# Performance work log

Hardware: AMD Instinct MI355X
Metric: run time of the kernel (lower is better)

## Reference

```python
import jax, jax.numpy as jnp
import numpy as np

B, N, D, S, ITERS = 64, 4096, 256, 8, 3
EPS_ATTN = 1e-8
EPS_LN = 1e-5


def layernorm(x, g, b):
    mu = jnp.mean(x, axis=-1, keepdims=True)
    var = jnp.mean(jnp.square(x - mu), axis=-1, keepdims=True)
    return (x - mu) * jax.lax.rsqrt(var + EPS_LN) * g + b


def setup_inputs() -> dict:
    key = jax.random.key(0)
    ks = jax.random.split(key, 12)
    inputs = jax.random.normal(ks[0], (B, N, D), jnp.float32)
    mask = jax.random.randint(ks[1], (B, N), 0, 2) == 1  # bool, True = masked out
    # xavier-normal init for slots parameter [S, D]
    slots_init = jax.random.normal(ks[2], (S, D), jnp.float32) * np.sqrt(2.0 / (S + D))
    w_std = np.sqrt(1.0 / D)
    Wq = jax.random.normal(ks[3], (D, D), jnp.float32) * w_std
    bq = jnp.zeros((D,), jnp.float32)
    Wk = jax.random.normal(ks[4], (D, D), jnp.float32) * w_std
    bk = jnp.zeros((D,), jnp.float32)
    Wv = jax.random.normal(ks[5], (D, D), jnp.float32) * w_std
    bv = jnp.zeros((D,), jnp.float32)
    W1 = jax.random.normal(ks[6], (D, D), jnp.float32) * w_std
    b1 = jnp.zeros((D,), jnp.float32)
    W2 = jax.random.normal(ks[7], (D, D), jnp.float32) * w_std
    b2 = jnp.zeros((D,), jnp.float32)
    g_in, b_in = jnp.ones((D,)), jnp.zeros((D,))
    g_s, b_s = jnp.ones((D,)), jnp.zeros((D,))
    g_m, b_m = jnp.ones((D,)), jnp.zeros((D,))
    g_o, b_o = jnp.ones((D,)), jnp.zeros((D,))
    return {
        "inputs": inputs, "mask": mask, "slots_init": slots_init,
        "g_in": g_in, "b_in": b_in, "g_s": g_s, "b_s": b_s,
        "g_m": g_m, "b_m": b_m, "g_o": g_o, "b_o": b_o,
        "Wq": Wq, "bq": bq, "Wk": Wk, "bk": bk, "Wv": Wv, "bv": bv,
        "W1": W1, "b1": b1, "W2": W2, "b2": b2,
    }


def reference(inputs, mask, slots_init, g_in, b_in, g_s, b_s, g_m, b_m, g_o, b_o,
              Wq, bq, Wk, bk, Wv, bv, W1, b1, W2, b2):
    x = layernorm(inputs, g_in, b_in)            # [B,N,D]
    k = x @ Wk + bk                               # [B,N,D]
    v = x @ Wv + bv                               # [B,N,D]
    slots = jnp.broadcast_to(slots_init, (B, S, D))
    scale = D ** -0.5
    neg_max = -jnp.finfo(inputs.dtype).max
    for _ in range(ITERS):
        slots_prev = slots
        s = layernorm(slots, g_s, b_s)
        q = s @ Wq + bq                           # [B,S,D]
        dots = jnp.einsum('bid,bjd->bij', q, k) * scale   # [B,S,N]
        dots = jnp.where(mask[:, None, :], neg_max, dots)
        attn = jax.nn.softmax(dots, axis=1)       # softmax over slots (unusual axis)
        attn = attn / (jnp.sum(attn, axis=-1, keepdims=True) + EPS_ATTN)
        updates = jnp.einsum('bjd,bij->bid', v, attn)     # [B,S,D]
        slots = slots_prev + updates
        h = layernorm(slots, g_m, b_m)
        h = jax.nn.relu(h @ W1 + b1) @ W2 + b2    # 2-layer MLP
        slots = slots + h
    return layernorm(slots, g_o, b_o)
```

## Files before the change

### kernel.cpp

```cpp
#include <hip/hip_runtime.h>
#include <stdint.h>

#define BB 64
#define NN 4096
#define DD 256
#define SS 8
#define NITER 3
#define NCHUNK 8
#define EPS_LN 1e-5f
#define EPS_ATTN 1e-8f

typedef __attribute__((ext_vector_type(4))) float fvec4;
typedef __attribute__((ext_vector_type(8))) __bf16 bf16x8;
typedef __attribute__((ext_vector_type(8))) unsigned short usvec8;
typedef __attribute__((ext_vector_type(4))) unsigned short usvec4;

__device__ __forceinline__ float bf2f(unsigned short u) {
  return __uint_as_float(((unsigned)u) << 16);
}
__device__ __forceinline__ unsigned short f2bf(float f) {
  unsigned u = __float_as_uint(f);
  u += 0x7FFFu + ((u >> 16) & 1u);
  return (unsigned short)(u >> 16);
}
__device__ __forceinline__ void async_copy16(void* ldsp, const void* gp) {
  __builtin_amdgcn_global_load_lds(
      (const __attribute__((address_space(1))) unsigned int*)gp,
      (__attribute__((address_space(3))) unsigned int*)ldsp, 16, 0, 0);
}

__global__ void k_sinit(const float* __restrict__ slots_init, float* __restrict__ slots) {
  int b = blockIdx.x, t = threadIdx.x;
  const fvec4* src = (const fvec4*)slots_init;
  fvec4* dst = (fvec4*)(slots + (size_t)b * SS * DD);
  for (int j = t; j < SS * DD / 4; j += 256) dst[j] = src[j];
}

__global__ void k_wprepT(const float* __restrict__ Wk, float* __restrict__ WkT) {
  __shared__ float tile[16][17];
  int bx = blockIdx.x, by = blockIdx.y, t = threadIdx.x;
  int r = t >> 4, c = t & 15;
  tile[r][c] = Wk[(size_t)(by * 16 + r) * DD + bx * 16 + c];
  __syncthreads();
  WkT[(size_t)(bx * 16 + r) * DD + by * 16 + c] = tile[c][r];
}

__launch_bounds__(256)
__global__ void k_wcomb(const float* __restrict__ Wq, const float* __restrict__ WkT,
                        const float* __restrict__ bq, const float* __restrict__ bk,
                        float* __restrict__ Wqk, float* __restrict__ bqk,
                        float* __restrict__ wqbk, float* __restrict__ bqbk) {
  __shared__ float wqrow[DD];
  __shared__ float red[4];
  const float sc = 0.0625f;
  int j = blockIdx.x, t = threadIdx.x;
  wqrow[t] = Wq[(size_t)j * DD + t];
  __syncthreads();
  float a = 0.f;
#pragma unroll 4
  for (int dk = 0; dk < DD; dk++) a += wqrow[dk] * WkT[(size_t)dk * DD + t];
  Wqk[(size_t)j * DD + t] = a * sc;
  float c = wqrow[t] * bk[t];
#pragma unroll
  for (int m = 32; m >= 1; m >>= 1) c += __shfl_xor(c, m);
  if ((t & 63) == 0) red[t >> 6] = c;
  __syncthreads();
  if (t == 0) wqbk[j] = sc * (red[0] + red[1] + red[2] + red[3]);
  if (j == 0) {
    float bb = 0.f;
#pragma unroll 4
    for (int dk = 0; dk < DD; dk++) bb += bq[dk] * WkT[(size_t)dk * DD + t];
    bqk[t] = bb * sc;
    __syncthreads();
    float c2 = bq[t] * bk[t];
#pragma unroll
    for (int m = 32; m >= 1; m >>= 1) c2 += __shfl_xor(c2, m);
    if ((t & 63) == 0) red[t >> 6] = c2;
    __syncthreads();
    if (t == 0) bqbk[0] = sc * (red[0] + red[1] + red[2] + red[3]);
  }
}

__launch_bounds__(256)
__global__ void k_lnx(const float* __restrict__ in, const float* __restrict__ g,
                      const float* __restrict__ bt, unsigned short* __restrict__ xbf) {
  int t = threadIdx.x;
  long row = (long)blockIdx.x * 32 + (t >> 3);
  int u = t & 7;
  const float* rp = in + row * DD;
  fvec4 v[8];
  float s = 0.f, s2 = 0.f;
#pragma unroll
  for (int j = 0; j < 8; j++) {
    v[j] = *(const fvec4*)(rp + j * 32 + u * 4);
    s += v[j].x + v[j].y + v[j].z + v[j].w;
    s2 += v[j].x * v[j].x + v[j].y * v[j].y + v[j].z * v[j].z + v[j].w * v[j].w;
  }
  s += __shfl_xor(s, 1); s2 += __shfl_xor(s2, 1);
  s += __shfl_xor(s, 2); s2 += __shfl_xor(s2, 2);
  s += __shfl_xor(s, 4); s2 += __shfl_xor(s2, 4);
  float mu = s / DD;
  float rs = rsqrtf(s2 / DD - mu * mu + EPS_LN);
#pragma unroll
  for (int j = 0; j < 8; j++) {
    fvec4 gg = *(const fvec4*)(g + j * 32 + u * 4);
    fvec4 bb = *(const fvec4*)(bt + j * 32 + u * 4);
    usvec4 o;
    o[0] = f2bf((v[j].x - mu) * rs * gg.x + bb.x);
    o[1] = f2bf((v[j].y - mu) * rs * gg.y + bb.y);
    o[2] = f2bf((v[j].z - mu) * rs * gg.z + bb.z);
    o[3] = f2bf((v[j].w - mu) * rs * gg.w + bb.w);
    *(usvec4*)&xbf[row * DD + j * 32 + u * 4] = o;
  }
}

__launch_bounds__(256)
__global__ void k_slotq2(const float* __restrict__ slots, const float* __restrict__ g_s,
                         const float* __restrict__ b_s, const float* __restrict__ Wqk,
                         const float* __restrict__ bqk, const float* __restrict__ wqbk,
                         const float* __restrict__ bqbk, float* __restrict__ qk,
                         float* __restrict__ qb, float* __restrict__ colsum) {
  __shared__ float sl[SS][DD];
  __shared__ float part[4][SS][64];
  __shared__ float qbp[4][SS];
  int b = blockIdx.x, cg = blockIdx.y, t = threadIdx.x;
  if (cg == 0 && t < SS) colsum[b * SS + t] = 0.f;
  int row = t >> 5, seg = t & 31;
  {
    const float* sp = slots + (size_t)(b * SS + row) * DD + seg * 8;
    float v[8];
    float s = 0.f, s2 = 0.f;
#pragma unroll
    for (int e = 0; e < 8; e++) { v[e] = sp[e]; s += v[e]; s2 += v[e] * v[e]; }
#pragma unroll
    for (int m = 16; m >= 1; m >>= 1) { s += __shfl_xor(s, m); s2 += __shfl_xor(s2, m); }
    float mu = s / DD;
    float rs = rsqrtf(s2 / DD - mu * mu + EPS_LN);
#pragma unroll
    for (int e = 0; e < 8; e++) {
      int d = seg * 8 + e;
      sl[row][d] = (v[e] - mu) * rs * g_s[d] + b_s[d];
    }
  }
  __syncthreads();
  float wb = wqbk[t];
  float c8[SS];
#pragma unroll
  for (int i = 0; i < SS; i++) c8[i] = sl[i][t] * wb;
#pragma unroll
  for (int m = 32; m >= 1; m >>= 1)
#pragma unroll
    for (int i = 0; i < SS; i++) c8[i] += __shfl_xor(c8[i], m);
  if ((t & 63) == 0) {
#pragma unroll
    for (int i = 0; i < SS; i++) qbp[t >> 6][i] = c8[i];
  }
  int kq = t >> 6, c = t & 63;
  int colg = cg * 64 + c;
  float a[SS] = {};
  for (int kk = 0; kk < 64; kk++) {
    int k = kq * 64 + kk;
    float wv = Wqk[(size_t)k * DD + colg];
#pragma unroll
    for (int i = 0; i < SS; i++) a[i] += sl[i][k] * wv;
  }
#pragma unroll
  for (int i = 0; i < SS; i++) part[kq][i][c] = a[i];
  __syncthreads();
  int i0 = t >> 6;
#pragma unroll
  for (int ii = 0; ii < 2; ii++) {
    int i = i0 + ii * 4;
    float s = part[0][i][c] + part[1][i][c] + part[2][i][c] + part[3][i][c];
    qk[(size_t)(b * SS + i) * DD + colg] = s + bqk[colg];
  }
  if (cg == 0 && t < SS)
    qb[b * SS + t] = qbp[0][t] + qbp[1][t] + qbp[2][t] + qbp[3][t] + bqbk[0];
}

__launch_bounds__(256, 2)
__global__ void k_attn2(const unsigned short* __restrict__ xbf,
                        const float* __restrict__ qkb, const float* __restrict__ qb,
                        const int* __restrict__ mask,
                        float* __restrict__ colsum, float* __restrict__ upart) {
  __shared__ __attribute__((aligned(16))) unsigned short kt[2][64 * 256];
  __shared__ float aL[2][64 * 9];
  int b = blockIdx.y, chunk = blockIdx.x, t = threadIdx.x;
  int w = t >> 6, lane = t & 63;
  int n_base = chunk * 512;
  int cl15 = lane & 15, hg = lane >> 4;

  bf16x8 qf[8];
  {
    int qrow = cl15 < 8 ? cl15 : 0;
    const float* qp = qkb + (size_t)(b * SS + qrow) * DD;
#pragma unroll
    for (int kst = 0; kst < 8; kst++) {
      int d0 = kst * 32 + hg * 8;
      usvec8 uq;
      if (cl15 < 8) {
        fvec4 q0 = *(const fvec4*)(qp + d0);
        fvec4 q1 = *(const fvec4*)(qp + d0 + 4);
        uq[0] = f2bf(q0.x); uq[1] = f2bf(q0.y); uq[2] = f2bf(q0.z); uq[3] = f2bf(q0.w);
        uq[4] = f2bf(q1.x); uq[5] = f2bf(q1.y); uq[6] = f2bf(q1.z); uq[7] = f2bf(q1.w);
      } else {
        uq = (usvec8)0;
      }
      qf[kst] = __builtin_bit_cast(bf16x8, uq);
    }
  }
  float qadd[4];
#pragma unroll
  for (int e = 0; e < 4; e++) qadd[e] = qb[b * SS + (hg & 1) * 4 + e];

  float acc[SS][8] = {};
  float csum[4] = {};
  int ns = t >> 5;

  auto stage = [&](int c, int bb) {
    int r0 = n_base + c * 64;
#pragma unroll
    for (int j = 0; j < 8; j++) {
      int gidx = w * 512 + j * 64 + lane;
      int row = gidx >> 5, c16 = gidx & 31;
      async_copy16(&kt[bb][gidx * 8],
                   xbf + ((size_t)(b * NN + r0 + row)) * DD + ((c16 ^ (row & 7)) * 8));
    }
  };

  stage(0, 0);
  for (int c = 0; c < 8; c++) {
    int bb = c & 1, pb = c & 1;
    int r0 = n_base + c * 64;
    if (c < 7) {
      stage(c + 1, bb ^ 1);
      asm volatile("s_waitcnt vmcnt(8)" ::: "memory");
    } else {
      asm volatile("s_waitcnt vmcnt(0)" ::: "memory");
    }
    __builtin_amdgcn_sched_barrier(0);
    fvec4 S = {0.f, 0.f, 0.f, 0.f};
    int row_l = w * 16 + cl15;
#pragma unroll
    for (int kst = 0; kst < 8; kst++) {
      int c16 = (kst * 4 + hg) ^ (row_l & 7);
      bf16x8 bfk = *(const bf16x8*)&kt[bb][row_l * 256 + c16 * 8];
      S = __builtin_amdgcn_mfma_f32_16x16x32_bf16(qf[kst], bfk, S, 0, 0, 0);
    }
    S[0] += qadd[0]; S[1] += qadd[1]; S[2] += qadd[2]; S[3] += qadd[3];
    {
      float m4 = fmaxf(fmaxf(S[0], S[1]), fmaxf(S[2], S[3]));
      float mo = __shfl_xor(m4, 16);
      float mx = fmaxf(m4, mo);
      float e0 = __expf(S[0] - mx), e1 = __expf(S[1] - mx);
      float e2 = __expf(S[2] - mx), e3 = __expf(S[3] - mx);
      float s4 = e0 + e1 + e2 + e3;
      float so = __shfl_xor(s4, 16);
      float inv = 1.f / (s4 + so);
      int mk = mask[(size_t)b * NN + r0 + row_l];
      float a0 = mk ? 0.125f : e0 * inv;
      float a1 = mk ? 0.125f : e1 * inv;
      float a2 = mk ? 0.125f : e2 * inv;
      float a3 = mk ? 0.125f : e3 * inv;
      if (lane < 32) {
        csum[0] += a0; csum[1] += a1; csum[2] += a2; csum[3] += a3;
        float* ap = &aL[pb][(w * 16 + cl15) * 9 + hg * 4];
        ap[0] = a0; ap[1] = a1; ap[2] = a2; ap[3] = a3;
      }
    }
    __syncthreads();
#pragma unroll
    for (int s8 = 0; s8 < 8; s8++) {
      int r = s8 * 8 + ns;
      usvec8 vv = *(const usvec8*)&kt[bb][r * 256 + (((t & 31)) ^ (r & 7)) * 8];
      float vf[8];
#pragma unroll
      for (int e = 0; e < 8; e++) vf[e] = bf2f(vv[e]);
#pragma unroll
      for (int i = 0; i < SS; i++) {
        float aw = aL[pb][r * 9 + i];
#pragma unroll
        for (int e = 0; e < 8; e++) acc[i][e] += aw * vf[e];
      }
    }
    __syncthreads();
  }
#pragma unroll
  for (int m = 1; m <= 8; m <<= 1)
#pragma unroll
    for (int e = 0; e < 4; e++) csum[e] += __shfl_xor(csum[e], m);
  if (lane == 0) {
#pragma unroll
    for (int e = 0; e < 4; e++) atomicAdd(&colsum[b * SS + e], csum[e]);
  } else if (lane == 16) {
#pragma unroll
    for (int e = 0; e < 4; e++) atomicAdd(&colsum[b * SS + 4 + e], csum[e]);
  }
#pragma unroll
  for (int i = 0; i < SS; i++)
#pragma unroll
    for (int e = 0; e < 8; e++) acc[i][e] += __shfl_xor(acc[i][e], 32);
  __syncthreads();
  float* red = (float*)&kt[0][0];
  if (lane < 32) {
#pragma unroll
    for (int i = 0; i < SS; i++) {
      fvec4 a0 = {acc[i][0], acc[i][1], acc[i][2], acc[i][3]};
      fvec4 a1 = {acc[i][4], acc[i][5], acc[i][6], acc[i][7]};
      *(fvec4*)&red[(w * SS + i) * DD + lane * 8] = a0;
      *(fvec4*)&red[(w * SS + i) * DD + lane * 8 + 4] = a1;
    }
  }
  __syncthreads();
  int i2 = t >> 5, dsg = (t & 31) * 8;
  float* up = upart + ((size_t)(b * NCHUNK + chunk)) * (SS * DD) + i2 * DD + dsg;
#pragma unroll
  for (int e = 0; e < 8; e++)
    up[e] = red[(0 * SS + i2) * DD + dsg + e] + red[(1 * SS + i2) * DD + dsg + e] +
            red[(2 * SS + i2) * DD + dsg + e] + red[(3 * SS + i2) * DD + dsg + e];
}

__launch_bounds__(256)
__global__ void k_updv(const float* __restrict__ upart, const float* __restrict__ Wv,
                       const float* __restrict__ bv, const float* __restrict__ colsum,
                       float* __restrict__ upd) {
  __shared__ float yL[SS][DD];
  __shared__ float part[4][SS][64];
  int b = blockIdx.x, cg = blockIdx.y, t = threadIdx.x;
#pragma unroll
  for (int i = 0; i < SS; i++) {
    float s = 0.f;
#pragma unroll
    for (int c = 0; c < NCHUNK; c++)
      s += upart[((size_t)(b * NCHUNK + c)) * (SS * DD) + i * DD + t];
    yL[i][t] = s;
  }
  __syncthreads();
  int kq = t >> 6, c = t & 63;
  int colg = cg * 64 + c;
  float a[SS] = {};
  for (int kk = 0; kk < 64; kk++) {
    int k = kq * 64 + kk;
    float wv = Wv[(size_t)k * DD + colg];
#pragma unroll
    for (int i = 0; i < SS; i++) a[i] += yL[i][k] * wv;
  }
#pragma unroll
  for (int i = 0; i < SS; i++) part[kq][i][c] = a[i];
  __syncthreads();
  int i0 = t >> 6;
  float bvc = bv[colg];
#pragma unroll
  for (int ii = 0; ii < 2; ii++) {
    int i = i0 + ii * 4;
    float s = part[0][i][c] + part[1][i][c] + part[2][i][c] + part[3][i][c];
    upd[(size_t)(b * SS + i) * DD + colg] = s + bvc * colsum[b * SS + i];
  }
}

__launch_bounds__(256)
__global__ void k_mlp1(const float* __restrict__ slots, const float* __restrict__ colsum,
                       const float* __restrict__ upd, const float* __restrict__ g_m,
                       const float* __restrict__ b_m, const float* __restrict__ W1,
                       const float* __restrict__ b1, float* __restrict__ h2g,
                       float* __restrict__ snbuf) {
  __shared__ float hL[SS][DD];
  __shared__ float part[4][SS][64];
  int b = blockIdx.x, cg = blockIdx.y, t = threadIdx.x;
  int row = t >> 5, seg = t & 31;
  {
    float inv = 1.0f / (colsum[b * SS + row] + EPS_ATTN);
    const float* sp = slots + (size_t)(b * SS + row) * DD + seg * 8;
    const float* up = upd + (size_t)(b * SS + row) * DD + seg * 8;
    float v[8];
    float s = 0.f, s2 = 0.f;
#pragma unroll
    for (int e = 0; e < 8; e++) {
      v[e] = sp[e] + up[e] * inv;
      s += v[e]; s2 += v[e] * v[e];
    }
    if (cg == 0) {
      float* snp = snbuf + (size_t)(b * SS + row) * DD + seg * 8;
#pragma unroll
      for (int e = 0; e < 8; e++) snp[e] = v[e];
    }
#pragma unroll
    for (int m = 16; m >= 1; m >>= 1) { s += __shfl_xor(s, m); s2 += __shfl_xor(s2, m); }
    float mu = s / DD;
    float rs = rsqrtf(s2 / DD - mu * mu + EPS_LN);
#pragma unroll
    for (int e = 0; e < 8; e++) {
      int d = seg * 8 + e;
      hL[row][d] = (v[e] - mu) * rs * g_m[d] + b_m[d];
    }
  }
  __syncthreads();
  int kq = t >> 6, c = t & 63;
  int colg = cg * 64 + c;
  float a[SS] = {};
  for (int kk = 0; kk < 64; kk++) {
    int k = kq * 64 + kk;
    float wv = W1[(size_t)k * DD + colg];
#pragma unroll
    for (int i = 0; i < SS; i++) a[i] += hL[i][k] * wv;
  }
#pragma unroll
  for (int i = 0; i < SS; i++) part[kq][i][c] = a[i];
  __syncthreads();
  int i0 = t >> 6;
#pragma unroll
  for (int ii = 0; ii < 2; ii++) {
    int i = i0 + ii * 4;
    float s = part[0][i][c] + part[1][i][c] + part[2][i][c] + part[3][i][c];
    h2g[(size_t)(b * SS + i) * DD + colg] = fmaxf(s + b1[colg], 0.f);
  }
}

__launch_bounds__(256)
__global__ void k_mlp2(float* __restrict__ slots, const float* __restrict__ snbuf,
                       const float* __restrict__ h2g, const float* __restrict__ W2,
                       const float* __restrict__ b2) {
  __shared__ float h2L[SS][DD];
  __shared__ float part[4][SS][64];
  int b = blockIdx.x, cg = blockIdx.y, t = threadIdx.x;
  {
    const fvec4* src = (const fvec4*)(h2g + (size_t)b * SS * DD);
    fvec4* dst = (fvec4*)h2L;
    for (int j = t; j < SS * DD / 4; j += 256) dst[j] = src[j];
  }
  __syncthreads();
  int kq = t >> 6, c = t & 63;
  int colg = cg * 64 + c;
  float a[SS] = {};
  for (int kk = 0; kk < 64; kk++) {
    int k = kq * 64 + kk;
    float wv = W2[(size_t)k * DD + colg];
#pragma unroll
    for (int i = 0; i < SS; i++) a[i] += h2L[i][k] * wv;
  }
#pragma unroll
  for (int i = 0; i < SS; i++) part[kq][i][c] = a[i];
  __syncthreads();
  int i0 = t >> 6;
#pragma unroll
  for (int ii = 0; ii < 2; ii++) {
    int i = i0 + ii * 4;
    float s = part[0][i][c] + part[1][i][c] + part[2][i][c] + part[3][i][c];
    size_t idx = (size_t)(b * SS + i) * DD + colg;
    slots[idx] = snbuf[idx] + s + b2[colg];
  }
}

__launch_bounds__(256)
__global__ void k_out(const float* __restrict__ slots, const float* __restrict__ g_o,
                      const float* __restrict__ b_o, float* __restrict__ out) {
  int b = blockIdx.x, t = threadIdx.x;
  int row = t >> 5, seg = t & 31;
  const float* sp = slots + (size_t)(b * SS + row) * DD + seg * 8;
  float v[8];
  float s = 0.f, s2 = 0.f;
#pragma unroll
  for (int e = 0; e < 8; e++) { v[e] = sp[e]; s += v[e]; s2 += v[e] * v[e]; }
#pragma unroll
  for (int m = 16; m >= 1; m >>= 1) { s += __shfl_xor(s, m); s2 += __shfl_xor(s2, m); }
  float mu = s / DD;
  float rs = rsqrtf(s2 / DD - mu * mu + EPS_LN);
#pragma unroll
  for (int e = 0; e < 8; e++) {
    int d = seg * 8 + e;
    out[(size_t)(b * SS + row) * DD + d] = (v[e] - mu) * rs * g_o[d] + b_o[d];
  }
}

extern "C" void kernel_launch(void* const* d_in, const int* in_sizes, int n_in,
                              void* d_out, int out_size, void* d_ws, size_t ws_size,
                              hipStream_t stream) {
  (void)in_sizes; (void)n_in; (void)out_size; (void)ws_size;
  const float* inputs = (const float*)d_in[0];
  const int* mask = (const int*)d_in[1];
  const float* slots_init = (const float*)d_in[2];
  const float* g_in = (const float*)d_in[3];
  const float* b_in = (const float*)d_in[4];
  const float* g_s = (const float*)d_in[5];
  const float* b_s = (const float*)d_in[6];
  const float* g_m = (const float*)d_in[7];
  const float* b_m = (const float*)d_in[8];
  const float* g_o = (const float*)d_in[9];
  const float* b_o = (const float*)d_in[10];
  const float* Wq = (const float*)d_in[11];
  const float* bq = (const float*)d_in[12];
  const float* Wk = (const float*)d_in[13];
  const float* bk = (const float*)d_in[14];
  const float* Wv = (const float*)d_in[15];
  const float* bv = (const float*)d_in[16];
  const float* W1 = (const float*)d_in[17];
  const float* b1 = (const float*)d_in[18];
  const float* W2 = (const float*)d_in[19];
  const float* b2 = (const float*)d_in[20];
  float* out = (float*)d_out;

  char* ws = (char*)d_ws;
  size_t off = 0;
  auto alloc = [&](size_t bytes) -> void* {
    void* p = ws + off;
    off += (bytes + 255) & ~(size_t)255;
    return p;
  };
  unsigned short* xbf = (unsigned short*)alloc((size_t)BB * NN * DD * 2);
  float* WkT = (float*)alloc((size_t)DD * DD * 4);
  float* Wqk = (float*)alloc((size_t)DD * DD * 4);
  float* bqk = (float*)alloc((size_t)DD * 4);
  float* wqbk = (float*)alloc((size_t)DD * 4);
  float* bqbk = (float*)alloc(4);
  float* qk = (float*)alloc((size_t)BB * SS * DD * 4);
  float* qb = (float*)alloc((size_t)BB * SS * 4);
  float* slots = (float*)alloc((size_t)BB * SS * DD * 4);
  float* snbuf = (float*)alloc((size_t)BB * SS * DD * 4);
  float* h2g = (float*)alloc((size_t)BB * SS * DD * 4);
  float* upd = (float*)alloc((size_t)BB * SS * DD * 4);
  float* upart = (float*)alloc((size_t)BB * NCHUNK * SS * DD * 4);
  float* colsum = (float*)alloc((size_t)BB * SS * 4);

  k_sinit<<<dim3(BB), dim3(256), 0, stream>>>(slots_init, slots);
  k_wprepT<<<dim3(16, 16), dim3(256), 0, stream>>>(Wk, WkT);
  k_wcomb<<<dim3(DD), dim3(256), 0, stream>>>(Wq, WkT, bq, bk, Wqk, bqk, wqbk, bqbk);
  k_lnx<<<dim3(BB * NN / 32), dim3(256), 0, stream>>>(inputs, g_in, b_in, xbf);

  for (int it = 0; it < NITER; ++it) {
    k_slotq2<<<dim3(BB, 4), dim3(256), 0, stream>>>(slots, g_s, b_s, Wqk, bqk, wqbk, bqbk,
                                                    qk, qb, colsum);
    k_attn2<<<dim3(NCHUNK, BB), dim3(256), 0, stream>>>(xbf, qk, qb, mask, colsum, upart);
    k_updv<<<dim3(BB, 4), dim3(256), 0, stream>>>(upart, Wv, bv, colsum, upd);
    k_mlp1<<<dim3(BB, 4), dim3(256), 0, stream>>>(slots, colsum, upd, g_m, b_m, W1, b1, h2g, snbuf);
    k_mlp2<<<dim3(BB, 4), dim3(256), 0, stream>>>(slots, snbuf, h2g, W2, b2);
  }
  k_out<<<dim3(BB), dim3(256), 0, stream>>>(slots, g_o, b_o, out);
}
```

Measured before the change: 426.5 us.

## Fuse Wv projection, MLP and next-iteration query into one slot-side kernel

Replaces four per-iteration kernels (updv, mlp1, mlp2, slotq2) with a single k_slotside kernel launched on a (BB,4) grid. Each block redundantly computes the full Wv, W1 and W2 products for its batch entry, then the query projection for its column group. Slot and colsum buffers are double-buffered so that blocks can read the previous state while block cg==0 writes the new one. This removes three launches per iteration and the global round-trips of the intermediate buffers, at the cost of each of the four column blocks repeating the full 256x256 matvecs, which quadruples the weight reads and FLOPs for these stages.

```diff
diff --git a/kernel.cpp b/kernel.cpp
--- a/kernel.cpp
+++ b/kernel.cpp
@@ -321,12 +321,25 @@
 }
 
 __launch_bounds__(256)
-__global__ void k_updv(const float* __restrict__ upart, const float* __restrict__ Wv,
-                       const float* __restrict__ bv, const float* __restrict__ colsum,
-                       float* __restrict__ upd) {
+__global__ void k_slotside(const float* __restrict__ slots_rd, float* __restrict__ slots_wr,
+                           const float* __restrict__ upart,
+                           const float* __restrict__ Wv, const float* __restrict__ bv,
+                           const float* __restrict__ colsum_rd, float* __restrict__ colsum_wr,
+                           const float* __restrict__ g_m, const float* __restrict__ b_m,
+                           const float* __restrict__ W1, const float* __restrict__ b1,
+                           const float* __restrict__ W2, const float* __restrict__ b2,
+                           const float* __restrict__ g_s, const float* __restrict__ b_s,
+                           const float* __restrict__ Wqk, const float* __restrict__ bqk,
+                           const float* __restrict__ wqbk, const float* __restrict__ bqbk,
+                           float* __restrict__ qk, float* __restrict__ qb, int do_q) {
   __shared__ float yL[SS][DD];
-  __shared__ float part[4][SS][64];
+  __shared__ float snL[SS][DD];
+  __shared__ float hL[SS][DD];
+  __shared__ float h2L[SS][DD];
+  __shared__ float qbp[4][SS];
   int b = blockIdx.x, cg = blockIdx.y, t = threadIdx.x;
+  int row = t >> 5, seg = t & 31;
+  float cs[SS], csinv[SS];
 #pragma unroll
   for (int i = 0; i < SS; i++) {
     float s = 0.f;
@@ -335,120 +348,130 @@
       s += upart[((size_t)(b * NCHUNK + c)) * (SS * DD) + i * DD + t];
     yL[i][t] = s;
   }
-  __syncthreads();
-  int kq = t >> 6, c = t & 63;
-  int colg = cg * 64 + c;
-  float a[SS] = {};
-  for (int kk = 0; kk < 64; kk++) {
-    int k = kq * 64 + kk;
-    float wv = Wv[(size_t)k * DD + colg];
-#pragma unroll
-    for (int i = 0; i < SS; i++) a[i] += yL[i][k] * wv;
-  }
-#pragma unroll
-  for (int i = 0; i < SS; i++) part[kq][i][c] = a[i];
+#pragma unroll
+  for (int i = 0; i < SS; i++) {
+    cs[i] = colsum_rd[b * SS + i];
+    csinv[i] = 1.f / (cs[i] + EPS_ATTN);
+  }
+  __syncthreads();
+  {
+    float acc[SS] = {};
+    for (int k = 0; k < DD; k += 4) {
+      float w0 = Wv[(size_t)(k + 0) * DD + t];
+      float w1 = Wv[(size_t)(k + 1) * DD + t];
+      float w2 = Wv[(size_t)(k + 2) * DD + t];
+      float w3 = Wv[(size_t)(k + 3) * DD + t];
+#pragma unroll
+      for (int i = 0; i < SS; i++)
+        acc[i] += yL[i][k] * w0 + yL[i][k + 1] * w1 + yL[i][k + 2] * w2 + yL[i][k + 3] * w3;
+    }
+    float bvt = bv[t];
+#pragma unroll
+    for (int i = 0; i < SS; i++)
+      snL[i][t] = slots_rd[(size_t)(b * SS + i) * DD + t] + (acc[i] + bvt * cs[i]) * csinv[i];
+  }
+  __syncthreads();
+  {
+    float v[8], s = 0.f, s2 = 0.f;
+#pragma unroll
+    for (int e = 0; e < 8; e++) { v[e] = snL[row][seg * 8 + e]; s += v[e]; s2 += v[e] * v[e]; }
+#pragma unroll
+    for (int m = 16; m >= 1; m >>= 1) { s += __shfl_xor(s, m); s2 += __shfl_xor(s2, m); }
+    float mu = s / DD, rs = rsqrtf(s2 / DD - mu * mu + EPS_LN);
+#pragma unroll
+    for (int e = 0; e < 8; e++) {
+      int d = seg * 8 + e;
+      hL[row][d] = (v[e] - mu) * rs * g_m[d] + b_m[d];
+    }
+  }
+  __syncthreads();
+  {
+    float acc[SS] = {};
+    for (int k = 0; k < DD; k += 4) {
+      float w0 = W1[(size_t)(k + 0) * DD + t];
+      float w1 = W1[(size_t)(k + 1) * DD + t];
+      float w2 = W1[(size_t)(k + 2) * DD + t];
+      float w3 = W1[(size_t)(k + 3) * DD + t];
+#pragma unroll
+      for (int i = 0; i < SS; i++)
+        acc[i] += hL[i][k] * w0 + hL[i][k + 1] * w1 + hL[i][k + 2] * w2 + hL[i][k + 3] * w3;
+    }
+    float b1t = b1[t];
+#pragma unroll
+    for (int i = 0; i < SS; i++) h2L[i][t] = fmaxf(acc[i] + b1t, 0.f);
+  }
+  __syncthreads();
+  {
+    float acc[SS] = {};
+    for (int k = 0; k < DD; k += 4) {
+      float w0 = W2[(size_t)(k + 0) * DD + t];
+      float w1 = W2[(size_t)(k + 1) * DD + t];
+      float w2 = W2[(size_t)(k + 2) * DD + t];
+      float w3 = W2[(size_t)(k + 3) * DD + t];
+#pragma unroll
+      for (int i = 0; i < SS; i++)
+        acc[i] += h2L[i][k] * w0 + h2L[i][k + 1] * w1 + h2L[i][k + 2] * w2 + h2L[i][k + 3] * w3;
+    }
+    float b2t = b2[t];
+#pragma unroll
+    for (int i = 0; i < SS; i++) {
+      float v = snL[i][t] + acc[i] + b2t;
+      yL[i][t] = v;
+      if (cg == 0) slots_wr[(size_t)(b * SS + i) * DD + t] = v;
+    }
+  }
+  if (cg == 0 && t < SS) colsum_wr[b * SS + t] = 0.f;
+  if (!do_q) return;
+  __syncthreads();
+  {
+    float v[8], s = 0.f, s2 = 0.f;
+#pragma unroll
+    for (int e = 0; e < 8; e++) { v[e] = yL[row][seg * 8 + e]; s += v[e]; s2 += v[e] * v[e]; }
+#pragma unroll
+    for (int m = 16; m >= 1; m >>= 1) { s += __shfl_xor(s, m); s2 += __shfl_xor(s2, m); }
+    float mu = s / DD, rs = rsqrtf(s2 / DD - mu * mu + EPS_LN);
+#pragma unroll
+    for (int e = 0; e < 8; e++) {
+      int d = seg * 8 + e;
+      snL[row][d] = (v[e] - mu) * rs * g_s[d] + b_s[d];
+    }
+  }
+  __syncthreads();
+  float wb = wqbk[t];
+  float c8[SS];
+#pragma unroll
+  for (int i = 0; i < SS; i++) c8[i] = snL[i][t] * wb;
+#pragma unroll
+  for (int m = 32; m >= 1; m >>= 1)
+#pragma unroll
+    for (int i = 0; i < SS; i++) c8[i] += __shfl_xor(c8[i], m);
+  if ((t & 63) == 0) {
+#pragma unroll
+    for (int i = 0; i < SS; i++) qbp[t >> 6][i] = c8[i];
+  }
+  float(*part)[SS][64] = (float(*)[SS][64]) & hL[0][0];
+  int kq = t >> 6, c = t & 63, colg = cg * 64 + c;
+  {
+    float a[SS] = {};
+    for (int kk = 0; kk < 64; kk++) {
+      int k = kq * 64 + kk;
+      float wv = Wqk[(size_t)k * DD + colg];
+#pragma unroll
+      for (int i = 0; i < SS; i++) a[i] += snL[i][k] * wv;
+    }
+#pragma unroll
+    for (int i = 0; i < SS; i++) part[kq][i][c] = a[i];
+  }
   __syncthreads();
   int i0 = t >> 6;
-  float bvc = bv[colg];
 #pragma unroll
   for (int ii = 0; ii < 2; ii++) {
     int i = i0 + ii * 4;
     float s = part[0][i][c] + part[1][i][c] + part[2][i][c] + part[3][i][c];
-    upd[(size_t)(b * SS + i) * DD + colg] = s + bvc * colsum[b * SS + i];
-  }
-}
-
-__launch_bounds__(256)
-__global__ void k_mlp1(const float* __restrict__ slots, const float* __restrict__ colsum,
-                       const float* __restrict__ upd, const float* __restrict__ g_m,
-                       const float* __restrict__ b_m, const float* __restrict__ W1,
-                       const float* __restrict__ b1, float* __restrict__ h2g,
-                       float* __restrict__ snbuf) {
-  __shared__ float hL[SS][DD];
-  __shared__ float part[4][SS][64];
-  int b = blockIdx.x, cg = blockIdx.y, t = threadIdx.x;
-  int row = t >> 5, seg = t & 31;
-  {
-    float inv = 1.0f / (colsum[b * SS + row] + EPS_ATTN);
-    const float* sp = slots + (size_t)(b * SS + row) * DD + seg * 8;
-    const float* up = upd + (size_t)(b * SS + row) * DD + seg * 8;
-    float v[8];
-    float s = 0.f, s2 = 0.f;
-#pragma unroll
-    for (int e = 0; e < 8; e++) {
-      v[e] = sp[e] + up[e] * inv;
-      s += v[e]; s2 += v[e] * v[e];
-    }
-    if (cg == 0) {
-      float* snp = snbuf + (size_t)(b * SS + row) * DD + seg * 8;
-#pragma unroll
-      for (int e = 0; e < 8; e++) snp[e] = v[e];
-    }
-#pragma unroll
-    for (int m = 16; m >= 1; m >>= 1) { s += __shfl_xor(s, m); s2 += __shfl_xor(s2, m); }
-    float mu = s / DD;
-    float rs = rsqrtf(s2 / DD - mu * mu + EPS_LN);
-#pragma unroll
-    for (int e = 0; e < 8; e++) {
-      int d = seg * 8 + e;
-      hL[row][d] = (v[e] - mu) * rs * g_m[d] + b_m[d];
-    }
-  }
-  __syncthreads();
-  int kq = t >> 6, c = t & 63;
-  int colg = cg * 64 + c;
-  float a[SS] = {};
-  for (int kk = 0; kk < 64; kk++) {
-    int k = kq * 64 + kk;
-    float wv = W1[(size_t)k * DD + colg];
-#pragma unroll
-    for (int i = 0; i < SS; i++) a[i] += hL[i][k] * wv;
-  }
-#pragma unroll
-  for (int i = 0; i < SS; i++) part[kq][i][c] = a[i];
-  __syncthreads();
-  int i0 = t >> 6;
-#pragma unroll
-  for (int ii = 0; ii < 2; ii++) {
-    int i = i0 + ii * 4;
-    float s = part[0][i][c] + part[1][i][c] + part[2][i][c] + part[3][i][c];
-    h2g[(size_t)(b * SS + i) * DD + colg] = fmaxf(s + b1[colg], 0.f);
-  }
-}
-
-__launch_bounds__(256)
-__global__ void k_mlp2(float* __restrict__ slots, const float* __restrict__ snbuf,
-                       const float* __restrict__ h2g, const float* __restrict__ W2,
-                       const float* __restrict__ b2) {
-  __shared__ float h2L[SS][DD];
-  __shared__ float part[4][SS][64];
-  int b = blockIdx.x, cg = blockIdx.y, t = threadIdx.x;
-  {
-    const fvec4* src = (const fvec4*)(h2g + (size_t)b * SS * DD);
-    fvec4* dst = (fvec4*)h2L;
-    for (int j = t; j < SS * DD / 4; j += 256) dst[j] = src[j];
-  }
-  __syncthreads();
-  int kq = t >> 6, c = t & 63;
-  int colg = cg * 64 + c;
-  float a[SS] = {};
-  for (int kk = 0; kk < 64; kk++) {
-    int k = kq * 64 + kk;
-    float wv = W2[(size_t)k * DD + colg];
-#pragma unroll
-    for (int i = 0; i < SS; i++) a[i] += h2L[i][k] * wv;
-  }
-#pragma unroll
-  for (int i = 0; i < SS; i++) part[kq][i][c] = a[i];
-  __syncthreads();
-  int i0 = t >> 6;
-#pragma unroll
-  for (int ii = 0; ii < 2; ii++) {
-    int i = i0 + ii * 4;
-    float s = part[0][i][c] + part[1][i][c] + part[2][i][c] + part[3][i][c];
-    size_t idx = (size_t)(b * SS + i) * DD + colg;
-    slots[idx] = snbuf[idx] + s + b2[colg];
-  }
+    qk[(size_t)(b * SS + i) * DD + colg] = s + bqk[colg];
+  }
+  if (cg == 0 && t < SS)
+    qb[b * SS + t] = qbp[0][t] + qbp[1][t] + qbp[2][t] + qbp[3][t] + bqbk[0];
 }
 
 __launch_bounds__(256)
@@ -514,25 +537,29 @@
   float* bqbk = (float*)alloc(4);
   float* qk = (float*)alloc((size_t)BB * SS * DD * 4);
   float* qb = (float*)alloc((size_t)BB * SS * 4);
-  float* slots = (float*)alloc((size_t)BB * SS * DD * 4);
-  float* snbuf = (float*)alloc((size_t)BB * SS * DD * 4);
-  float* h2g = (float*)alloc((size_t)BB * SS * DD * 4);
-  float* upd = (float*)alloc((size_t)BB * SS * DD * 4);
+  float* slots = (float*)alloc((size_t)2 * BB * SS * DD * 4);
   float* upart = (float*)alloc((size_t)BB * NCHUNK * SS * DD * 4);
-  float* colsum = (float*)alloc((size_t)BB * SS * 4);
+  float* colsum = (float*)alloc((size_t)2 * BB * SS * 4);
+
+  const size_t SLOT_SZ = (size_t)BB * SS * DD;
+  const size_t CS_SZ = (size_t)BB * SS;
 
   k_sinit<<<dim3(BB), dim3(256), 0, stream>>>(slots_init, slots);
   k_wprepT<<<dim3(16, 16), dim3(256), 0, stream>>>(Wk, WkT);
   k_wcomb<<<dim3(DD), dim3(256), 0, stream>>>(Wq, WkT, bq, bk, Wqk, bqk, wqbk, bqbk);
   k_lnx<<<dim3(BB * NN / 32), dim3(256), 0, stream>>>(inputs, g_in, b_in, xbf);
+  k_slotq2<<<dim3(BB, 4), dim3(256), 0, stream>>>(slots, g_s, b_s, Wqk, bqk, wqbk, bqbk,
+                                                  qk, qb, colsum);
 
   for (int it = 0; it < NITER; ++it) {
-    k_slotq2<<<dim3(BB, 4), dim3(256), 0, stream>>>(slots, g_s, b_s, Wqk, bqk, wqbk, bqbk,
-                                                    qk, qb, colsum);
-    k_attn2<<<dim3(NCHUNK, BB), dim3(256), 0, stream>>>(xbf, qk, qb, mask, colsum, upart);
-    k_updv<<<dim3(BB, 4), dim3(256), 0, stream>>>(upart, Wv, bv, colsum, upd);
-    k_mlp1<<<dim3(BB, 4), dim3(256), 0, stream>>>(slots, colsum, upd, g_m, b_m, W1, b1, h2g, snbuf);
-    k_mlp2<<<dim3(BB, 4), dim3(256), 0, stream>>>(slots, snbuf, h2g, W2, b2);
-  }
-  k_out<<<dim3(BB), dim3(256), 0, stream>>>(slots, g_o, b_o, out);
-}
+    float* cs_rd = colsum + (it & 1) * CS_SZ;
+    float* cs_wr = colsum + ((it + 1) & 1) * CS_SZ;
+    float* sl_rd = slots + (it & 1) * SLOT_SZ;
+    float* sl_wr = slots + ((it + 1) & 1) * SLOT_SZ;
+    k_attn2<<<dim3(NCHUNK, BB), dim3(256), 0, stream>>>(xbf, qk, qb, mask, cs_rd, upart);
+    k_slotside<<<dim3(BB, 4), dim3(256), 0, stream>>>(
+        sl_rd, sl_wr, upart, Wv, bv, cs_rd, cs_wr, g_m, b_m, W1, b1, W2, b2,
+        g_s, b_s, Wqk, bqk, wqbk, bqbk, qk, qb, it < NITER - 1 ? 1 : 0);
+  }
+  k_out<<<dim3(BB), dim3(256), 0, stream>>>(slots + SLOT_SZ, g_o, b_o, out);
+}
```

After: 568.6 us. 1.33x slower.
